# Kernel optimization log

Measured on AMD Instinct MI355X. Metric: run time of the kernel, lower is better.

## Reference

```python
import jax, jax.numpy as jnp
import numpy as np

INPUT_DIM = 1024
NUM_HEADS = 16
HEAD_DIM = INPUT_DIM // NUM_HEADS


def setup_inputs() -> dict:
    key = jax.random.key(0)
    k1, k2, k3 = jax.random.split(key, 3)
    x = jax.random.normal(k1, (4, 2048, INPUT_DIM), dtype=jnp.float32)
    # nn.Linear(input_dim, 3*input_dim): weight [3D, D], bias [3D]
    bound = 1.0 / np.sqrt(INPUT_DIM)
    W_qkv = jax.random.uniform(k2, (3 * INPUT_DIM, INPUT_DIM), dtype=jnp.float32, minval=-bound, maxval=bound)
    b_qkv = jax.random.uniform(k3, (3 * INPUT_DIM,), dtype=jnp.float32, minval=-bound, maxval=bound)
    return {"x": x, "W_qkv": W_qkv, "b_qkv": b_qkv}


def reference(x, W_qkv, b_qkv):
    b, t, d = x.shape
    # fused QKV projection: [b,t,3D]
    qkv = jnp.einsum('btd,ed->bte', x, W_qkv) + b_qkv
    qkv = qkv.reshape(b, t, 3, NUM_HEADS, HEAD_DIM)
    q = qkv[:, :, 0].transpose(0, 2, 1, 3)  # [b,h,t,hd]
    k = qkv[:, :, 1].transpose(0, 2, 1, 3)
    v = qkv[:, :, 2].transpose(0, 2, 1, 3)
    scale = 1.0 / np.sqrt(HEAD_DIM).astype(np.float32)
    scores = jnp.einsum('bhqd,bhkd->bhqk', q, k) * scale
    attn = jax.nn.softmax(scores, axis=-1)
    out = jnp.einsum('bhqk,bhkd->bhqd', attn, v)
    return out.transpose(0, 2, 1, 3).reshape(b, t, d)
```

## Files before the change

kernel.cpp:

```cpp
#include <hip/hip_runtime.h>


#define NBH   64
#define L2E   1.44269504088896340736f

typedef __bf16 bf16x8 __attribute__((ext_vector_type(8)));
typedef float  f32x4  __attribute__((ext_vector_type(4)));

static __device__ __forceinline__ unsigned short bf1(float a) {
    union { __bf16 h; unsigned short u; } t; t.h = (__bf16)a; return t.u;
}
static __device__ __forceinline__ unsigned pk2(float a, float b) {
    union { __bf16 h[2]; unsigned u; } t;
    t.h[0] = (__bf16)a; t.h[1] = (__bf16)b; return t.u;
}

static __device__ __forceinline__ void gload16(const unsigned short* g, unsigned short* l) {
    __builtin_amdgcn_global_load_lds(
        (const __attribute__((address_space(1))) unsigned int*)g,
        (__attribute__((address_space(3))) unsigned int*)l, 16, 0, 0);
}

__global__ __launch_bounds__(256) void convert_bf16(
    const float* __restrict__ x, const float* __restrict__ W,
    unsigned short* __restrict__ xb, unsigned short* __restrict__ wb)
{
    const int NX = (8192 * 1024) / 8;
    const int NW = (3072 * 1024) / 8;
    int stride = gridDim.x * blockDim.x;
    for (int c = blockIdx.x * blockDim.x + threadIdx.x; c < NX + NW; c += stride) {
        const float* src; unsigned short* dst; int cc;
        if (c < NX) { src = x; dst = xb; cc = c; }
        else        { src = W; dst = wb; cc = c - NX; }
        float4 a = *(const float4*)(src + (size_t)cc * 8);
        float4 b = *(const float4*)(src + (size_t)cc * 8 + 4);
        uint4 v;
        v.x = pk2(a.x, a.y); v.y = pk2(a.z, a.w);
        v.z = pk2(b.x, b.y); v.w = pk2(b.z, b.w);
        *(uint4*)(dst + (size_t)cc * 8) = v;
    }
}

__global__ __launch_bounds__(256) void qkv_gemm(
    const unsigned short* __restrict__ xb, const unsigned short* __restrict__ wb,
    const float* __restrict__ bias,
    unsigned short* __restrict__ qw, unsigned short* __restrict__ kw,
    unsigned short* __restrict__ vtw)
{
    __shared__ __align__(16) unsigned short As[128 * 64];
    __shared__ __align__(16) unsigned short Bs[128 * 64];

    int bid = blockIdx.x;
    int swz = (bid & 7) * 192 + (bid >> 3);
    int tm = swz & 63, tn = swz >> 6;
    int brow = tm * 128, bcol = tn * 128;

    int tid = threadIdx.x, l = tid & 63, wid = tid >> 6;
    int wr = wid >> 1, wc = wid & 1;

    f32x4 acc[4][4] = {};

    for (int k0 = 0; k0 < 1024; k0 += 64) {
        __syncthreads();
#pragma unroll
        for (int i = 0; i < 4; i++) {
            int cb = i * 256 + wid * 64;
            int ca = cb + l;
            int row = ca >> 3, c8 = ca & 7;
            gload16(xb + (size_t)(brow + row) * 1024 + k0 + c8 * 8, &As[cb * 8]);
            gload16(wb + (size_t)(bcol + row) * 1024 + k0 + c8 * 8, &Bs[cb * 8]);
        }
        asm volatile("s_waitcnt vmcnt(0)" ::: "memory");
        __syncthreads();

        bf16x8 aF[4][2], bF[4][2];
#pragma unroll
        for (int m = 0; m < 4; m++) {
            int row = wr * 64 + m * 16 + (l & 15);
#pragma unroll
            for (int kb = 0; kb < 2; kb++)
                aF[m][kb] = *(const bf16x8*)((const char*)As + row * 128 + kb * 64 + (l >> 4) * 16);
        }
#pragma unroll
        for (int n = 0; n < 4; n++) {
            int row = wc * 64 + n * 16 + (l & 15);
#pragma unroll
            for (int kb = 0; kb < 2; kb++)
                bF[n][kb] = *(const bf16x8*)((const char*)Bs + row * 128 + kb * 64 + (l >> 4) * 16);
        }
#pragma unroll
        for (int kb = 0; kb < 2; kb++)
#pragma unroll
            for (int m = 0; m < 4; m++)
#pragma unroll
                for (int n = 0; n < 4; n++)
                    acc[m][n] = __builtin_amdgcn_mfma_f32_16x16x32_bf16(
                        aF[m][kb], bF[n][kb], acc[m][n], 0, 0, 0);
    }

#pragma unroll
    for (int n = 0; n < 4; n++) {
        int e = bcol + wc * 64 + n * 16 + (l & 15);
        float bv = bias[e];
        int which = e >> 10;
        int h = (e >> 6) & 15;
        int hd = e & 63;
#pragma unroll
        for (int m = 0; m < 4; m++) {
#pragma unroll
            for (int r = 0; r < 4; r++) {
                int M = brow + wr * 64 + m * 16 + (l >> 4) * 4 + r;
                int bb = M >> 11, t = M & 2047;
                int bh = bb * 16 + h;
                float ov = acc[m][n][r] + bv;
                if (which == 0) ov *= 0.125f;
                unsigned short val = bf1(ov);
                if (which == 0)
                    qw[((size_t)bh * 2048 + t) * 64 + hd] = val;
                else if (which == 1)
                    kw[((size_t)bh * 2048 + t) * 64 + hd] = val;
                else
                    vtw[((size_t)bh * 64 + hd) * 2048 + t] = val;
            }
        }
    }
}

static __device__ __forceinline__ int Lperm(int p) {
    int n = p >> 4, gg = (p >> 2) & 3, rr = p & 3;
    return ((n & 1) << 5) | (gg << 3) | ((n >> 1) << 2) | rr;
}

__global__ __launch_bounds__(256) void attn(
    const unsigned short* __restrict__ qw, const unsigned short* __restrict__ kw,
    const unsigned short* __restrict__ vtw, float* __restrict__ out)
{
    __shared__ __align__(16) unsigned short Ks[64 * 64];
    __shared__ __align__(16) unsigned short Vs[64 * 64];

    int bid = blockIdx.x;
    int bh = bid >> 5, qt = bid & 31;
    int tid = threadIdx.x, w = tid >> 6, l = tid & 63;
    int g = l >> 4, q = l & 15;

    const unsigned short* Qb = qw  + (size_t)bh * 2048 * 64;
    const unsigned short* Kb = kw  + (size_t)bh * 2048 * 64;
    const unsigned short* Vb = vtw + (size_t)bh * 64 * 2048;

    int q0 = qt * 64 + w * 16;

    bf16x8 bQ[2];
#pragma unroll
    for (int kb = 0; kb < 2; kb++)
        bQ[kb] = *(const bf16x8*)(Qb + (size_t)(q0 + q) * 64 + kb * 32 + g * 8);

    f32x4 o[4] = {};
    float mL = -1e30f, lrun = 0.f;

    int srow = tid >> 3, sseg = tid & 7;
    const unsigned short* kSrc0 = Kb + (size_t)Lperm(srow)      * 64 + sseg * 8;
    const unsigned short* kSrc1 = Kb + (size_t)Lperm(srow + 32) * 64 + sseg * 8;
    const unsigned short* vSrc0 = Vb + (size_t)srow        * 2048 + sseg * 8;
    const unsigned short* vSrc1 = Vb + (size_t)(srow + 32) * 2048 + sseg * 8;
    int off0 = srow * 128        + ((sseg * 16) ^ ((srow & 7) << 4));
    int off1 = (srow + 32) * 128 + ((sseg * 16) ^ ((srow & 7) << 4));

    uint4 rk0 = *(const uint4*)(kSrc0);
    uint4 rk1 = *(const uint4*)(kSrc1);
    uint4 rv0 = *(const uint4*)(vSrc0);
    uint4 rv1 = *(const uint4*)(vSrc1);

    for (int kt = 0; kt < 32; kt++) {
        __syncthreads();
        *(uint4*)((char*)Ks + off0) = rk0;
        *(uint4*)((char*)Ks + off1) = rk1;
        *(uint4*)((char*)Vs + off0) = rv0;
        *(uint4*)((char*)Vs + off1) = rv1;
        __syncthreads();
        if (kt < 31) {
            size_t kAdv = (size_t)(kt + 1) * 64 * 64;
            int    vAdv = (kt + 1) * 64;
            rk0 = *(const uint4*)(kSrc0 + kAdv);
            rk1 = *(const uint4*)(kSrc1 + kAdv);
            rv0 = *(const uint4*)(vSrc0 + vAdv);
            rv1 = *(const uint4*)(vSrc1 + vAdv);
        }

        f32x4 s[4];
#pragma unroll
        for (int n = 0; n < 4; n++) {
            int row = n * 16 + q;
            int sw = (row & 7) << 4;
            f32x4 z = {};
#pragma unroll
            for (int kb = 0; kb < 2; kb++) {
                bf16x8 aK = *(const bf16x8*)((const char*)Ks + row * 128 + ((kb * 64 + g * 16) ^ sw));
                z = __builtin_amdgcn_mfma_f32_16x16x32_bf16(aK, bQ[kb], z, 0, 0, 0);
            }
            s[n] = z;
        }

        float m0 = fmaxf(fmaxf(s[0][0], s[0][1]), fmaxf(s[0][2], s[0][3]));
        float m1 = fmaxf(fmaxf(s[1][0], s[1][1]), fmaxf(s[1][2], s[1][3]));
        float m2 = fmaxf(fmaxf(s[2][0], s[2][1]), fmaxf(s[2][2], s[2][3]));
        float m3 = fmaxf(fmaxf(s[3][0], s[3][1]), fmaxf(s[3][2], s[3][3]));
        float smax = fmaxf(fmaxf(m0, m1), fmaxf(m2, m3));
        smax = fmaxf(smax, __shfl_xor(smax, 16));
        smax = fmaxf(smax, __shfl_xor(smax, 32));
        float tL = smax * L2E;

        if (!__all(tL <= mL + 8.0f)) {
            float mnewL = fmaxf(mL, tL);
            float c = __builtin_amdgcn_exp2f(mL - mnewL);
            mL = mnewL;
            lrun *= c;
#pragma unroll
            for (int r = 0; r < 4; r++) {
                float cr = __shfl(c, 20 * g + r);
#pragma unroll
                for (int df = 0; df < 4; df++) o[df][r] *= cr;
            }
        }

        unsigned Wp[4][2];
        float tsum = 0.f;
#pragma unroll
        for (int n = 0; n < 4; n++) {
            float p0 = __builtin_amdgcn_exp2f(__builtin_fmaf(s[n][0], L2E, -mL));
            float p1 = __builtin_amdgcn_exp2f(__builtin_fmaf(s[n][1], L2E, -mL));
            float p2 = __builtin_amdgcn_exp2f(__builtin_fmaf(s[n][2], L2E, -mL));
            float p3 = __builtin_amdgcn_exp2f(__builtin_fmaf(s[n][3], L2E, -mL));
            tsum += (p0 + p1) + (p2 + p3);
            Wp[n][0] = pk2(p0, p1);
            Wp[n][1] = pk2(p2, p3);
        }
        tsum += __shfl_xor(tsum, 16);
        tsum += __shfl_xor(tsum, 32);
        lrun += tsum;

        union { unsigned u[4]; bf16x8 v; } ap0, ap1;
        ap0.u[0] = Wp[0][0]; ap0.u[1] = Wp[0][1]; ap0.u[2] = Wp[2][0]; ap0.u[3] = Wp[2][1];
        ap1.u[0] = Wp[1][0]; ap1.u[1] = Wp[1][1]; ap1.u[2] = Wp[3][0]; ap1.u[3] = Wp[3][1];

#pragma unroll
        for (int df = 0; df < 4; df++) {
            int vrow = df * 16 + q;
            int sw = (vrow & 7) << 4;
            bf16x8 bV0 = *(const bf16x8*)((const char*)Vs + vrow * 128 + ((g * 16) ^ sw));
            bf16x8 bV1 = *(const bf16x8*)((const char*)Vs + vrow * 128 + ((64 + g * 16) ^ sw));
            o[df] = __builtin_amdgcn_mfma_f32_16x16x32_bf16(ap0.v, bV0, o[df], 0, 0, 0);
            o[df] = __builtin_amdgcn_mfma_f32_16x16x32_bf16(ap1.v, bV1, o[df], 0, 0, 0);
        }
    }

    float linv[4];
#pragma unroll
    for (int r = 0; r < 4; r++)
        linv[r] = 1.0f / __shfl(lrun, 20 * g + r);
    int b = bh >> 4, h = bh & 15;
#pragma unroll
    for (int df = 0; df < 4; df++)
#pragma unroll
        for (int r = 0; r < 4; r++)
            out[(size_t)(b * 2048 + q0 + 4 * g + r) * 1024 + h * 64 + df * 16 + q] = o[df][r] * linv[r];
}

extern "C" void kernel_launch(void* const* d_in, const int* in_sizes, int n_in,
                              void* d_out, int out_size, void* d_ws, size_t ws_size,
                              hipStream_t stream)
{
    const float* x    = (const float*)d_in[0];
    const float* W    = (const float*)d_in[1];
    const float* bqkv = (const float*)d_in[2];
    float* out = (float*)d_out;

    unsigned short* xb = (unsigned short*)d_out;
    unsigned short* qw = (unsigned short*)d_ws;
    unsigned short* kw = qw + (size_t)NBH * 2048 * 64;
    unsigned short* vt = kw + (size_t)NBH * 2048 * 64;
    unsigned short* wb = vt + (size_t)NBH * 64 * 2048;

    convert_bf16<<<2048, 256, 0, stream>>>(x, W, xb, wb);
    qkv_gemm<<<1536, 256, 0, stream>>>(xb, wb, bqkv, qw, kw, vt);
    attn<<<2048, 256, 0, stream>>>(qw, kw, vt, out);
}
```

Measured before the change: 314.4 us.

## Double-buffer QKV GEMM with swizzled LDS, fold log2e into Q, MFMA row sums

The QKV GEMM now double-buffers its LDS tiles, prefetching the next K-slice via global_load_lds while computing the current one. It also XOR-swizzles the LDS layout to avoid bank conflicts. Q is pre-scaled by log2(e) in the GEMM epilogue so the attention kernel can drop the per-element FMA. The softmax row sum is computed with an extra MFMA against a ones vector instead of adds and cross-lane shuffles. The cost is twice the LDS use (lower occupancy), and the row sum now uses the bf16-rounded probabilities.

```diff
diff --git a/kernel.cpp b/kernel.cpp
--- a/kernel.cpp
+++ b/kernel.cpp
@@ -47,8 +47,8 @@
     unsigned short* __restrict__ qw, unsigned short* __restrict__ kw,
     unsigned short* __restrict__ vtw)
 {
-    __shared__ __align__(16) unsigned short As[128 * 64];
-    __shared__ __align__(16) unsigned short Bs[128 * 64];
+    __shared__ __align__(16) unsigned short As[2][128 * 64];
+    __shared__ __align__(16) unsigned short Bs[2][128 * 64];
 
     int bid = blockIdx.x;
     int swz = (bid & 7) * 192 + (bid >> 3);
@@ -58,36 +58,65 @@
     int tid = threadIdx.x, l = tid & 63, wid = tid >> 6;
     int wr = wid >> 1, wc = wid & 1;
 
+    size_t aoff[4], boff[4];
+    int cbv[4];
+#pragma unroll
+    for (int i = 0; i < 4; i++) {
+        int cb = i * 256 + wid * 64;
+        int ca = cb + l;
+        int row = ca >> 3;
+        int c8 = (ca & 7) ^ (row & 7);
+        cbv[i]  = cb * 8;
+        aoff[i] = (size_t)(brow + row) * 1024 + c8 * 8;
+        boff[i] = (size_t)(bcol + row) * 1024 + c8 * 8;
+    }
+
     f32x4 acc[4][4] = {};
 
-    for (int k0 = 0; k0 < 1024; k0 += 64) {
-        __syncthreads();
-#pragma unroll
-        for (int i = 0; i < 4; i++) {
-            int cb = i * 256 + wid * 64;
-            int ca = cb + l;
-            int row = ca >> 3, c8 = ca & 7;
-            gload16(xb + (size_t)(brow + row) * 1024 + k0 + c8 * 8, &As[cb * 8]);
-            gload16(wb + (size_t)(bcol + row) * 1024 + k0 + c8 * 8, &Bs[cb * 8]);
-        }
-        asm volatile("s_waitcnt vmcnt(0)" ::: "memory");
-        __syncthreads();
-
+#pragma unroll
+    for (int i = 0; i < 4; i++) {
+        gload16(xb + aoff[i], &As[0][cbv[i]]);
+        gload16(wb + boff[i], &Bs[0][cbv[i]]);
+    }
+
+    for (int t = 0; t < 16; t++) {
+        int cur = t & 1;
+        if (t < 15) {
+            int k0 = (t + 1) * 64;
+#pragma unroll
+            for (int i = 0; i < 4; i++) {
+                gload16(xb + aoff[i] + k0, &As[cur ^ 1][cbv[i]]);
+                gload16(wb + boff[i] + k0, &Bs[cur ^ 1][cbv[i]]);
+            }
+            asm volatile("s_waitcnt vmcnt(8)" ::: "memory");
+        } else {
+            asm volatile("s_waitcnt vmcnt(0)" ::: "memory");
+        }
+        __builtin_amdgcn_s_barrier();
+
+        const char* Ab = (const char*)As[cur];
+        const char* Bb = (const char*)Bs[cur];
         bf16x8 aF[4][2], bF[4][2];
 #pragma unroll
         for (int m = 0; m < 4; m++) {
             int row = wr * 64 + m * 16 + (l & 15);
+            int sw = (row & 7) << 4;
 #pragma unroll
             for (int kb = 0; kb < 2; kb++)
-                aF[m][kb] = *(const bf16x8*)((const char*)As + row * 128 + kb * 64 + (l >> 4) * 16);
+                aF[m][kb] = *(const bf16x8*)(Ab + row * 128 + ((kb * 64 + (l >> 4) * 16) ^ sw));
         }
 #pragma unroll
         for (int n = 0; n < 4; n++) {
             int row = wc * 64 + n * 16 + (l & 15);
+            int sw = (row & 7) << 4;
 #pragma unroll
             for (int kb = 0; kb < 2; kb++)
-                bF[n][kb] = *(const bf16x8*)((const char*)Bs + row * 128 + kb * 64 + (l >> 4) * 16);
-        }
+                bF[n][kb] = *(const bf16x8*)(Bb + row * 128 + ((kb * 64 + (l >> 4) * 16) ^ sw));
+        }
+        asm volatile("s_waitcnt lgkmcnt(0)" ::: "memory");
+        __builtin_amdgcn_sched_barrier(0);
+        __builtin_amdgcn_s_barrier();
+
 #pragma unroll
         for (int kb = 0; kb < 2; kb++)
 #pragma unroll
@@ -113,7 +142,7 @@
                 int bb = M >> 11, t = M & 2047;
                 int bh = bb * 16 + h;
                 float ov = acc[m][n][r] + bv;
-                if (which == 0) ov *= 0.125f;
+                if (which == 0) ov *= 0.125f * L2E;
                 unsigned short val = bf1(ov);
                 if (which == 0)
                     qw[((size_t)bh * 2048 + t) * 64 + hd] = val;
@@ -154,8 +183,13 @@
     for (int kb = 0; kb < 2; kb++)
         bQ[kb] = *(const bf16x8*)(Qb + (size_t)(q0 + q) * 64 + kb * 32 + g * 8);
 
+    union { unsigned u[4]; bf16x8 v; } ones;
+#pragma unroll
+    for (int i = 0; i < 4; i++) ones.u[i] = 0x3F803F80u;
+
     f32x4 o[4] = {};
-    float mL = -1e30f, lrun = 0.f;
+    f32x4 lac = {};
+    float mL = -1e30f;
 
     int srow = tid >> 3, sseg = tid & 7;
     const unsigned short* kSrc0 = Kb + (size_t)Lperm(srow)      * 64 + sseg * 8;
@@ -200,47 +234,47 @@
             s[n] = z;
         }
 
-        float m0 = fmaxf(fmaxf(s[0][0], s[0][1]), fmaxf(s[0][2], s[0][3]));
-        float m1 = fmaxf(fmaxf(s[1][0], s[1][1]), fmaxf(s[1][2], s[1][3]));
-        float m2 = fmaxf(fmaxf(s[2][0], s[2][1]), fmaxf(s[2][2], s[2][3]));
-        float m3 = fmaxf(fmaxf(s[3][0], s[3][1]), fmaxf(s[3][2], s[3][3]));
-        float smax = fmaxf(fmaxf(m0, m1), fmaxf(m2, m3));
-        smax = fmaxf(smax, __shfl_xor(smax, 16));
-        smax = fmaxf(smax, __shfl_xor(smax, 32));
-        float tL = smax * L2E;
+        float t0 = fmaxf(fmaxf(s[0][0], s[0][1]), s[0][2]);
+        float t1 = fmaxf(fmaxf(s[0][3], s[1][0]), s[1][1]);
+        float t2 = fmaxf(fmaxf(s[1][2], s[1][3]), s[2][0]);
+        float t3 = fmaxf(fmaxf(s[2][1], s[2][2]), s[2][3]);
+        float t4 = fmaxf(fmaxf(s[3][0], s[3][1]), s[3][2]);
+        float u0 = fmaxf(fmaxf(t0, t1), t2);
+        float u1 = fmaxf(fmaxf(t3, t4), s[3][3]);
+        float tL = fmaxf(u0, u1);
+        tL = fmaxf(tL, __shfl_xor(tL, 16));
+        tL = fmaxf(tL, __shfl_xor(tL, 32));
 
         if (!__all(tL <= mL + 8.0f)) {
             float mnewL = fmaxf(mL, tL);
             float c = __builtin_amdgcn_exp2f(mL - mnewL);
             mL = mnewL;
-            lrun *= c;
 #pragma unroll
             for (int r = 0; r < 4; r++) {
                 float cr = __shfl(c, 20 * g + r);
+                lac[r] *= cr;
 #pragma unroll
                 for (int df = 0; df < 4; df++) o[df][r] *= cr;
             }
         }
 
         unsigned Wp[4][2];
-        float tsum = 0.f;
 #pragma unroll
         for (int n = 0; n < 4; n++) {
-            float p0 = __builtin_amdgcn_exp2f(__builtin_fmaf(s[n][0], L2E, -mL));
-            float p1 = __builtin_amdgcn_exp2f(__builtin_fmaf(s[n][1], L2E, -mL));
-            float p2 = __builtin_amdgcn_exp2f(__builtin_fmaf(s[n][2], L2E, -mL));
-            float p3 = __builtin_amdgcn_exp2f(__builtin_fmaf(s[n][3], L2E, -mL));
-            tsum += (p0 + p1) + (p2 + p3);
+            float p0 = __builtin_amdgcn_exp2f(s[n][0] - mL);
+            float p1 = __builtin_amdgcn_exp2f(s[n][1] - mL);
+            float p2 = __builtin_amdgcn_exp2f(s[n][2] - mL);
+            float p3 = __builtin_amdgcn_exp2f(s[n][3] - mL);
             Wp[n][0] = pk2(p0, p1);
             Wp[n][1] = pk2(p2, p3);
         }
-        tsum += __shfl_xor(tsum, 16);
-        tsum += __shfl_xor(tsum, 32);
-        lrun += tsum;
 
         union { unsigned u[4]; bf16x8 v; } ap0, ap1;
         ap0.u[0] = Wp[0][0]; ap0.u[1] = Wp[0][1]; ap0.u[2] = Wp[2][0]; ap0.u[3] = Wp[2][1];
         ap1.u[0] = Wp[1][0]; ap1.u[1] = Wp[1][1]; ap1.u[2] = Wp[3][0]; ap1.u[3] = Wp[3][1];
+
+        lac = __builtin_amdgcn_mfma_f32_16x16x32_bf16(ap0.v, ones.v, lac, 0, 0, 0);
+        lac = __builtin_amdgcn_mfma_f32_16x16x32_bf16(ap1.v, ones.v, lac, 0, 0, 0);
 
 #pragma unroll
         for (int df = 0; df < 4; df++) {
@@ -253,10 +287,9 @@
         }
     }
 
-    float linv[4];
-#pragma unroll
-    for (int r = 0; r < 4; r++)
-        linv[r] = 1.0f / __shfl(lrun, 20 * g + r);
+    f32x4 linv;
+#pragma unroll
+    for (int r = 0; r < 4; r++) linv[r] = 1.0f / lac[r];
     int b = bh >> 4, h = bh & 15;
 #pragma unroll
     for (int df = 0; df < 4; df++)
```

Measured after the change: 302.0 us. -3.9%, faster.
